# Kernel tuning notes

Measured on AMD Instinct MI355X. Metric: run time of the kernel, lower is better.

The kernel has to match this reference:

```python
import jax, jax.numpy as jnp
import numpy as np

ALPHA = 0.1      # weight on repulsion loss
NN_SIZE = 5      # k for knn (includes self, first neighbor dropped)
RADIUS = 0.07
H = 0.03
EPS = 1e-12


def _pairwise_sq(a, b):
    # a: (B, N, 3), b: (B, M, 3) -> (B, N, M) squared euclidean distances
    na = jnp.sum(a * a, axis=-1)[:, :, None]
    nb = jnp.sum(b * b, axis=-1)[:, None, :]
    return na + nb - 2.0 * jnp.einsum('bnc,bmc->bnm', a, b)


def setup_inputs() -> dict:
    key = jax.random.key(0)
    k1, k2, k3 = jax.random.split(key, 3)
    B, N = 8, 4096
    pred = jax.random.normal(k1, (B, N, 3), dtype=jnp.float32)
    gt = jax.random.normal(k2, (B, N, 3), dtype=jnp.float32)
    pcd_radius = jax.random.uniform(k3, (B, 1), dtype=jnp.float32)
    return {"pred": pred, "gt": gt, "pcd_radius": pcd_radius}


def reference(pred, gt, pcd_radius):
    # ---- Chamfer distance term (squared dists, as in ChamferDistance cuda op) ----
    d2 = _pairwise_sq(gt, pred)                  # (B, Ngt, Npred)
    cost_for = jnp.min(d2, axis=2)               # gt -> pred, (B, Ngt)
    cost_bac = jnp.min(d2, axis=1)               # pred -> gt, (B, Npred)
    cost = (0.8 * cost_for + 0.2 * cost_bac) / pcd_radius
    cd_loss = jnp.mean(cost)

    # ---- Repulsion (uniformity) term ----
    dpp = _pairwise_sq(pred, pred)               # (B, N, N)
    _, idx = jax.lax.top_k(-dpp, NN_SIZE)        # k nearest, (B, N, K); self is first
    idx = idx[:, :, 1:]                          # drop self, (B, N, K-1)
    # gather neighbors: (B, N, K-1, 3)
    neigh = jnp.take_along_axis(pred[:, None, :, :], idx[..., None], axis=2)
    diff = neigh - pred[:, :, None, :]
    dist2 = jnp.maximum(jnp.sum(diff * diff, axis=-1), EPS)  # (B, N, K-1)
    dist = jnp.sqrt(dist2)
    weight = jnp.exp(-dist2 / (H * H))
    uniform_loss = jnp.mean((RADIUS - dist) * weight)

    return cd_loss + ALPHA * uniform_loss
```

## Files before the change

### kernel.cpp

```cpp
#include <hip/hip_runtime.h>
#include <math.h>

#define THREADS 256
#define NWAVE 4
#define QB 128
#define TILE 1024
#define KSPLIT 2

#define MED3 __builtin_amdgcn_fmed3f

#define INS5(L0,L1,L2,L3,L4,C) do { float c_=(C);              \
    float n0_=fminf(L0,c_);                                    \
    float n1_=MED3(L0,L1,c_);                                  \
    float n2_=MED3(L1,L2,c_);                                  \
    float n3_=MED3(L2,L3,c_);                                  \
    float n4_=MED3(L3,L4,c_);                                  \
    L0=n0_; L1=n1_; L2=n2_; L3=n3_; L4=n4_; } while (0)

__device__ __forceinline__ float cdist(float qx,float qy,float qz,float4 t) {
    return fmaf(qx, t.x, fmaf(qy, t.y, fmaf(qz, t.z, t.w)));
}

__global__ __launch_bounds__(THREADS) void scan_kernel(
    const float* __restrict__ pred, const float* __restrict__ gt,
    const float* __restrict__ radius, float* __restrict__ acc,
    float* __restrict__ knnPart, int B, int N, int chunks, int knnItems)
{
    __shared__ float4 tile[TILE];
    __shared__ float part[NWAVE][QB][5];
    __shared__ float red[NWAVE];

    const float FLT_INF = 3.4e38f;

    int w = threadIdx.x >> 6, l = threadIdx.x & 63;

    int role, b, chunk, split = 0, tBegin, tEnd;
    if ((int)blockIdx.x < knnItems) {
        role = 2;
        int u = blockIdx.x;
        split = u % KSPLIT; u /= KSPLIT;
        chunk = u % chunks; b = u / chunks;
        int seg = (N + KSPLIT - 1) / KSPLIT;
        tBegin = split * seg; tEnd = min(tBegin + seg, N);
    } else {
        int u = blockIdx.x - knnItems;
        int perRole = B * chunks;
        role = u / perRole; u %= perRole;
        chunk = u % chunks; b = u / chunks;
        tBegin = 0; tEnd = N;
    }

    int qi0 = chunk * QB + l;
    int qi1 = qi0 + 64;
    const float* qb = (((role == 0) ? gt : pred)) + (size_t)b * N * 3;
    const float* tb = (((role == 1) ? gt : pred)) + (size_t)b * N * 3;

    float ax = 0.f, ay = 0.f, az = 0.f, bx = 0.f, by = 0.f, bz = 0.f;
    if (qi0 < N) { ax = qb[qi0*3]; ay = qb[qi0*3+1]; az = qb[qi0*3+2]; }
    if (qi1 < N) { bx = qb[qi1*3]; by = qb[qi1*3+1]; bz = qb[qi1*3+2]; }

    float mA0 = FLT_INF, mA1 = FLT_INF, mB0 = FLT_INF, mB1 = FLT_INF;
    float e0=FLT_INF,e1=FLT_INF,e2=FLT_INF,e3=FLT_INF,e4=FLT_INF;
    float o0=FLT_INF,o1=FLT_INF,o2=FLT_INF,o3=FLT_INF,o4=FLT_INF;

    for (int t0 = tBegin; t0 < tEnd; t0 += TILE) {
        int cnt = min(TILE, tEnd - t0);
        for (int k = threadIdx.x; k < cnt; k += THREADS) {
            float x = tb[(size_t)(t0 + k) * 3 + 0];
            float y = tb[(size_t)(t0 + k) * 3 + 1];
            float z = tb[(size_t)(t0 + k) * 3 + 2];
            float nb = fmaf(x, x, fmaf(y, y, z * z));
            tile[k] = make_float4(-2.f * x, -2.f * y, -2.f * z, nb);
        }
        __syncthreads();

        int seg = (cnt + NWAVE - 1) / NWAVE;
        int jb = w * seg, je = min(jb + seg, cnt);

        if (role < 2) {
            int j = jb;
            for (; j + 4 <= je; j += 4) {
                float4 t0v = tile[j], t1v = tile[j+1], t2v = tile[j+2], t3v = tile[j+3];
                mA0 = fminf(mA0, cdist(ax,ay,az,t0v));
                mB0 = fminf(mB0, cdist(bx,by,bz,t0v));
                mA1 = fminf(mA1, cdist(ax,ay,az,t1v));
                mB1 = fminf(mB1, cdist(bx,by,bz,t1v));
                mA0 = fminf(mA0, cdist(ax,ay,az,t2v));
                mB0 = fminf(mB0, cdist(bx,by,bz,t2v));
                mA1 = fminf(mA1, cdist(ax,ay,az,t3v));
                mB1 = fminf(mB1, cdist(bx,by,bz,t3v));
            }
            for (; j < je; ++j) {
                float4 t = tile[j];
                mA0 = fminf(mA0, cdist(ax,ay,az,t));
                mB0 = fminf(mB0, cdist(bx,by,bz,t));
            }
        } else {
            int j = jb;
            for (; j + 2 <= je; j += 2) {
                float4 t0v = tile[j], t1v = tile[j+1];
                float cA0 = cdist(ax,ay,az,t0v), cB0 = cdist(bx,by,bz,t0v);
                float cA1 = cdist(ax,ay,az,t1v), cB1 = cdist(bx,by,bz,t1v);
                INS5(e0,e1,e2,e3,e4, cA0);
                INS5(o0,o1,o2,o3,o4, cB0);
                INS5(e0,e1,e2,e3,e4, cA1);
                INS5(o0,o1,o2,o3,o4, cB1);
            }
            for (; j < je; ++j) {
                float4 t = tile[j];
                INS5(e0,e1,e2,e3,e4, cdist(ax,ay,az,t));
                INS5(o0,o1,o2,o3,o4, cdist(bx,by,bz,t));
            }
        }
        __syncthreads();
    }

    if (role < 2) {
        part[w][l][0]      = fminf(mA0, mA1);
        part[w][l + 64][0] = fminf(mB0, mB1);
    } else {
        part[w][l][0]=e0; part[w][l][1]=e1; part[w][l][2]=e2;
        part[w][l][3]=e3; part[w][l][4]=e4;
        part[w][l+64][0]=o0; part[w][l+64][1]=o1; part[w][l+64][2]=o2;
        part[w][l+64][3]=o3; part[w][l+64][4]=o4;
    }
    __syncthreads();

    if (role < 2) {
        float contrib = 0.f;
        if (threadIdx.x < QB) {
            int t = threadIdx.x;
            int q = chunk * QB + t;
            if (q < N) {
                float x = qb[q*3], y = qb[q*3+1], z = qb[q*3+2];
                float na = fmaf(x,x,fmaf(y,y,z*z));
                float best = fminf(fminf(part[0][t][0], part[1][t][0]),
                                   fminf(part[2][t][0], part[3][t][0]));
                float wgt = (role == 0) ? 0.8f : 0.2f;
                contrib = wgt * (na + best) / radius[b];
            }
        }
        #pragma unroll
        for (int off = 32; off > 0; off >>= 1) contrib += __shfl_down(contrib, off, 64);
        if (l == 0) red[w] = contrib;
        __syncthreads();
        if (threadIdx.x == 0) atomicAdd(&acc[0], red[0]+red[1]+red[2]+red[3]);
    } else {
        if (threadIdx.x < QB) {
            int t = threadIdx.x;
            int q = chunk * QB + t;
            if (q < N) {
                float s0=FLT_INF,s1=FLT_INF,s2=FLT_INF,s3=FLT_INF,s4=FLT_INF;
                #pragma unroll
                for (int ww = 0; ww < NWAVE; ++ww)
                    #pragma unroll
                    for (int k = 0; k < 5; ++k)
                        INS5(s0,s1,s2,s3,s4, part[ww][t][k]);
                float* kp = &knnPart[(((size_t)b * N + q) * KSPLIT + split) * 5];
                kp[0]=s0; kp[1]=s1; kp[2]=s2; kp[3]=s3; kp[4]=s4;
            }
        }
    }
}

__global__ __launch_bounds__(THREADS) void mergeB_kernel(
    const float* __restrict__ pred, const float* __restrict__ knnPart,
    float* __restrict__ acc, int B, int N)
{
    const float FLT_INF = 3.4e38f;
    const float RADIUS = 0.07f;
    const float INV_H2 = 1.0f / (0.03f * 0.03f);
    const float EPSV = 1e-12f;

    __shared__ float redu[NWAVE];

    int gid = blockIdx.x * THREADS + threadIdx.x;
    int BN = B * N;
    float uni = 0.f;

    if (gid < BN) {
        const float* qp = pred + (size_t)gid * 3;
        float x = qp[0], y = qp[1], z = qp[2];
        float na = fmaf(x,x,fmaf(y,y,z*z));
        const float* kp = &knnPart[(size_t)gid * KSPLIT * 5];
        float s0=FLT_INF,s1=FLT_INF,s2=FLT_INF,s3=FLT_INF,s4=FLT_INF;
        #pragma unroll
        for (int k = 0; k < KSPLIT * 5; ++k) INS5(s0,s1,s2,s3,s4, kp[k]);
        float ss[4] = {s1, s2, s3, s4};
        #pragma unroll
        for (int k = 0; k < 4; ++k) {
            float d2 = fmaxf(na + ss[k], EPSV);
            uni += (RADIUS - sqrtf(d2)) * __expf(-d2 * INV_H2);
        }
    }

    int w = threadIdx.x >> 6, l = threadIdx.x & 63;
    #pragma unroll
    for (int off = 32; off > 0; off >>= 1) uni += __shfl_down(uni, off, 64);
    if (l == 0) redu[w] = uni;
    __syncthreads();
    if (threadIdx.x == 0)
        atomicAdd(&acc[1], redu[0]+redu[1]+redu[2]+redu[3]);
}

__device__ __forceinline__ float sdist(float qx,float qy,float qz,float4 t) {
    return fmaf(-2.f, fmaf(qx,t.x,fmaf(qy,t.y,qz*t.z)), t.w);
}
__global__ __launch_bounds__(THREADS) void mono_kernel(
    const float* __restrict__ pred, const float* __restrict__ gt,
    const float* __restrict__ radius, float* __restrict__ acc,
    int B, int N, int chunksPerBatch)
{
    __shared__ float4 tgt[2048];
    __shared__ float part[NWAVE][128][5];
    __shared__ float naArr[128];
    __shared__ float red[NWAVE];
    const float FLT_INF = 3.4e38f;
    const float RADIUS = 0.07f;
    const float INV_H2 = 1.0f / (0.03f * 0.03f);
    const float EPSV = 1e-12f;

    int blocksPerRole = B * chunksPerBatch;
    int role  = blockIdx.x / blocksPerRole;
    int rem   = blockIdx.x % blocksPerRole;
    int b     = rem / chunksPerBatch;
    int chunk = rem % chunksPerBatch;
    int w = threadIdx.x >> 6, l = threadIdx.x & 63;
    int qi0 = chunk * 128 + l, qi1 = qi0 + 64;
    const float* qb = (((role == 0) ? gt : pred)) + (size_t)b * N * 3;
    const float* tb = (((role == 1) ? gt : pred)) + (size_t)b * N * 3;
    float q0x=0,q0y=0,q0z=0,q1x=0,q1y=0,q1z=0;
    if (qi0 < N) { q0x=qb[qi0*3]; q0y=qb[qi0*3+1]; q0z=qb[qi0*3+2]; }
    if (qi1 < N) { q1x=qb[qi1*3]; q1y=qb[qi1*3+1]; q1z=qb[qi1*3+2]; }
    float na0 = fmaf(q0x,q0x,fmaf(q0y,q0y,q0z*q0z));
    float na1 = fmaf(q1x,q1x,fmaf(q1y,q1y,q1z*q1z));
    if (w == 0) { naArr[l] = na0; naArr[l+64] = na1; }
    float mA=FLT_INF,mB=FLT_INF;
    float e0=FLT_INF,e1=FLT_INF,e2=FLT_INF,e3=FLT_INF,e4=FLT_INF;
    float o0=FLT_INF,o1=FLT_INF,o2=FLT_INF,o3=FLT_INF,o4=FLT_INF;
    for (int t0 = 0; t0 < N; t0 += 2048) {
        int cnt = min(2048, N - t0);
        for (int k = threadIdx.x; k < cnt; k += THREADS) {
            float x = tb[(size_t)(t0+k)*3], y = tb[(size_t)(t0+k)*3+1], z = tb[(size_t)(t0+k)*3+2];
            tgt[k] = make_float4(x,y,z,fmaf(x,x,fmaf(y,y,z*z)));
        }
        __syncthreads();
        int segsz = (cnt + NWAVE - 1)/NWAVE;
        int jb = w*segsz, je = min(jb+segsz, cnt);
        if (role < 2) {
            for (int j = jb; j < je; ++j) {
                float4 t = tgt[j];
                mA = fminf(mA, sdist(q0x,q0y,q0z,t));
                mB = fminf(mB, sdist(q1x,q1y,q1z,t));
            }
        } else {
            for (int j = jb; j < je; ++j) {
                float4 t = tgt[j];
                INS5(e0,e1,e2,e3,e4, sdist(q0x,q0y,q0z,t));
                INS5(o0,o1,o2,o3,o4, sdist(q1x,q1y,q1z,t));
            }
        }
        __syncthreads();
    }
    if (role < 2) { part[w][l][0]=mA; part[w][l+64][0]=mB; }
    else {
        part[w][l][0]=e0; part[w][l][1]=e1; part[w][l][2]=e2; part[w][l][3]=e3; part[w][l][4]=e4;
        part[w][l+64][0]=o0; part[w][l+64][1]=o1; part[w][l+64][2]=o2; part[w][l+64][3]=o3; part[w][l+64][4]=o4;
    }
    __syncthreads();
    float contrib = 0.f;
    int t = threadIdx.x;
    if (t < 128) {
        int q = chunk*128 + t;
        if (q < N) {
            float inv_r = 1.0f / radius[b];
            float na = naArr[t];
            if (role < 2) {
                float best = fminf(fminf(part[0][t][0],part[1][t][0]),
                                   fminf(part[2][t][0],part[3][t][0]));
                contrib = ((role==0)?0.8f:0.2f) * inv_r * (na + best);
            } else {
                float s0=FLT_INF,s1=FLT_INF,s2=FLT_INF,s3=FLT_INF,s4=FLT_INF;
                #pragma unroll
                for (int ww = 0; ww < NWAVE; ++ww)
                    #pragma unroll
                    for (int k = 0; k < 5; ++k)
                        INS5(s0,s1,s2,s3,s4, part[ww][t][k]);
                float ss[4] = {s1,s2,s3,s4};
                float s = 0.f;
                #pragma unroll
                for (int k = 0; k < 4; ++k) {
                    float d2 = fmaxf(na + ss[k], EPSV);
                    s += (RADIUS - sqrtf(d2)) * __expf(-d2 * INV_H2);
                }
                contrib = s;
            }
        }
    }
    #pragma unroll
    for (int off = 32; off > 0; off >>= 1) contrib += __shfl_down(contrib, off, 64);
    if (l == 0) red[w] = contrib;
    __syncthreads();
    if (threadIdx.x == 0)
        atomicAdd(&acc[role < 2 ? 0 : 1], red[0]+red[1]+red[2]+red[3]);
}

__global__ void upsample_final_kernel(const float* __restrict__ acc,
                                      float* __restrict__ out,
                                      float invCd, float invUni)
{
    out[0] = fmaf(acc[0], invCd, 0.1f * acc[1] * invUni);
}

extern "C" void kernel_launch(void* const* d_in, const int* in_sizes, int n_in,
                              void* d_out, int out_size, void* d_ws, size_t ws_size,
                              hipStream_t stream) {
    const float* pred   = (const float*)d_in[0];
    const float* gt     = (const float*)d_in[1];
    const float* radius = (const float*)d_in[2];
    float* out = (float*)d_out;
    float* acc = (float*)d_ws;

    int B = in_sizes[2];
    int N = in_sizes[0] / (3 * B);
    size_t BN = (size_t)B * N;

    hipMemsetAsync(acc, 0, 2 * sizeof(float), stream);

    size_t knnBytes = BN * KSPLIT * 5 * sizeof(float);
    size_t need = 64 + knnBytes;

    if (ws_size >= need) {
        float* knnPart = (float*)((char*)d_ws + 64);
        int chunks = (N + QB - 1) / QB;
        int knnItems  = B * chunks * KSPLIT;
        int chamItems = 2 * B * chunks;
        scan_kernel<<<knnItems + chamItems, THREADS, 0, stream>>>(
            pred, gt, radius, acc, knnPart, B, N, chunks, knnItems);
        int mb = (int)((BN + THREADS - 1) / THREADS);
        mergeB_kernel<<<mb, THREADS, 0, stream>>>(pred, knnPart, acc, B, N);
    } else {
        int chunksPerBatch = (N + 127) / 128;
        int blocks = 3 * B * chunksPerBatch;
        mono_kernel<<<blocks, THREADS, 0, stream>>>(pred, gt, radius, acc,
                                                    B, N, chunksPerBatch);
    }

    float invCd  = 1.0f / ((float)B * (float)N);
    float invUni = 1.0f / ((float)B * (float)N * 4.0f);
    upsample_final_kernel<<<1, 1, 0, stream>>>(acc, out, invCd, invUni);
}
```

Baseline: 72.93 us.

## Split chamfer and kNN target ranges further and merge partials in second kernel

Each chamfer query chunk now scans its targets in two halves, and kNN scans in four parts instead of two, which multiplies the number of scan blocks. Per-split chamfer minima go to a workspace buffer, and the merge kernel now also combines chamfer partials, applies the weights and radius, and reduces them. Tile size and the inner unroll are halved. The aim is more blocks to fill the GPU's compute units and shorter per-block scans, at the cost of extra global writes and a bigger merge pass.

```diff
diff --git a/kernel.cpp b/kernel.cpp
--- a/kernel.cpp
+++ b/kernel.cpp
@@ -4,8 +4,9 @@
 #define THREADS 256
 #define NWAVE 4
 #define QB 128
-#define TILE 1024
-#define KSPLIT 2
+#define TILE 512
+#define KSPLIT 4
+#define CSPLIT 2
 
 #define MED3 __builtin_amdgcn_fmed3f
 
@@ -23,18 +24,16 @@
 
 __global__ __launch_bounds__(THREADS) void scan_kernel(
     const float* __restrict__ pred, const float* __restrict__ gt,
-    const float* __restrict__ radius, float* __restrict__ acc,
-    float* __restrict__ knnPart, int B, int N, int chunks, int knnItems)
+    float* __restrict__ chamPart, float* __restrict__ knnPart,
+    int B, int N, int chunks, int knnItems)
 {
     __shared__ float4 tile[TILE];
     __shared__ float part[NWAVE][QB][5];
-    __shared__ float red[NWAVE];
 
     const float FLT_INF = 3.4e38f;
-
     int w = threadIdx.x >> 6, l = threadIdx.x & 63;
 
-    int role, b, chunk, split = 0, tBegin, tEnd;
+    int role, b, chunk, split, tBegin, tEnd;
     if ((int)blockIdx.x < knnItems) {
         role = 2;
         int u = blockIdx.x;
@@ -44,16 +43,19 @@
         tBegin = split * seg; tEnd = min(tBegin + seg, N);
     } else {
         int u = blockIdx.x - knnItems;
-        int perRole = B * chunks;
+        int perRole = B * chunks * CSPLIT;
         role = u / perRole; u %= perRole;
+        split = u % CSPLIT; u /= CSPLIT;
         chunk = u % chunks; b = u / chunks;
-        tBegin = 0; tEnd = N;
-    }
+        int seg = (N + CSPLIT - 1) / CSPLIT;
+        tBegin = split * seg; tEnd = min(tBegin + seg, N);
+    }
+
+    const float* qb = (((role == 0) ? gt : pred)) + (size_t)b * N * 3;
+    const float* tb = (((role == 1) ? gt : pred)) + (size_t)b * N * 3;
 
     int qi0 = chunk * QB + l;
     int qi1 = qi0 + 64;
-    const float* qb = (((role == 0) ? gt : pred)) + (size_t)b * N * 3;
-    const float* tb = (((role == 1) ? gt : pred)) + (size_t)b * N * 3;
 
     float ax = 0.f, ay = 0.f, az = 0.f, bx = 0.f, by = 0.f, bz = 0.f;
     if (qi0 < N) { ax = qb[qi0*3]; ay = qb[qi0*3+1]; az = qb[qi0*3+2]; }
@@ -69,8 +71,7 @@
             float x = tb[(size_t)(t0 + k) * 3 + 0];
             float y = tb[(size_t)(t0 + k) * 3 + 1];
             float z = tb[(size_t)(t0 + k) * 3 + 2];
-            float nb = fmaf(x, x, fmaf(y, y, z * z));
-            tile[k] = make_float4(-2.f * x, -2.f * y, -2.f * z, nb);
+            tile[k] = make_float4(-2.f*x, -2.f*y, -2.f*z, fmaf(x,x,fmaf(y,y,z*z)));
         }
         __syncthreads();
 
@@ -79,18 +80,14 @@
 
         if (role < 2) {
             int j = jb;
-            for (; j + 4 <= je; j += 4) {
-                float4 t0v = tile[j], t1v = tile[j+1], t2v = tile[j+2], t3v = tile[j+3];
+            for (; j + 2 <= je; j += 2) {
+                float4 t0v = tile[j], t1v = tile[j+1];
                 mA0 = fminf(mA0, cdist(ax,ay,az,t0v));
                 mB0 = fminf(mB0, cdist(bx,by,bz,t0v));
                 mA1 = fminf(mA1, cdist(ax,ay,az,t1v));
                 mB1 = fminf(mB1, cdist(bx,by,bz,t1v));
-                mA0 = fminf(mA0, cdist(ax,ay,az,t2v));
-                mB0 = fminf(mB0, cdist(bx,by,bz,t2v));
-                mA1 = fminf(mA1, cdist(ax,ay,az,t3v));
-                mB1 = fminf(mB1, cdist(bx,by,bz,t3v));
-            }
-            for (; j < je; ++j) {
+            }
+            if (j < je) {
                 float4 t = tile[j];
                 mA0 = fminf(mA0, cdist(ax,ay,az,t));
                 mB0 = fminf(mB0, cdist(bx,by,bz,t));
@@ -106,7 +103,7 @@
                 INS5(e0,e1,e2,e3,e4, cA1);
                 INS5(o0,o1,o2,o3,o4, cB1);
             }
-            for (; j < je; ++j) {
+            if (j < je) {
                 float4 t = tile[j];
                 INS5(e0,e1,e2,e3,e4, cdist(ax,ay,az,t));
                 INS5(o0,o1,o2,o3,o4, cdist(bx,by,bz,t));
@@ -126,30 +123,15 @@
     }
     __syncthreads();
 
-    if (role < 2) {
-        float contrib = 0.f;
-        if (threadIdx.x < QB) {
-            int t = threadIdx.x;
-            int q = chunk * QB + t;
-            if (q < N) {
-                float x = qb[q*3], y = qb[q*3+1], z = qb[q*3+2];
-                float na = fmaf(x,x,fmaf(y,y,z*z));
+    if (threadIdx.x < QB) {
+        int t = threadIdx.x;
+        int q = chunk * QB + t;
+        if (q < N) {
+            if (role < 2) {
                 float best = fminf(fminf(part[0][t][0], part[1][t][0]),
                                    fminf(part[2][t][0], part[3][t][0]));
-                float wgt = (role == 0) ? 0.8f : 0.2f;
-                contrib = wgt * (na + best) / radius[b];
-            }
-        }
-        #pragma unroll
-        for (int off = 32; off > 0; off >>= 1) contrib += __shfl_down(contrib, off, 64);
-        if (l == 0) red[w] = contrib;
-        __syncthreads();
-        if (threadIdx.x == 0) atomicAdd(&acc[0], red[0]+red[1]+red[2]+red[3]);
-    } else {
-        if (threadIdx.x < QB) {
-            int t = threadIdx.x;
-            int q = chunk * QB + t;
-            if (q < N) {
+                chamPart[(((size_t)role * B + b) * N + q) * CSPLIT + split] = best;
+            } else {
                 float s0=FLT_INF,s1=FLT_INF,s2=FLT_INF,s3=FLT_INF,s4=FLT_INF;
                 #pragma unroll
                 for (int ww = 0; ww < NWAVE; ++ww)
@@ -164,7 +146,9 @@
 }
 
 __global__ __launch_bounds__(THREADS) void mergeB_kernel(
-    const float* __restrict__ pred, const float* __restrict__ knnPart,
+    const float* __restrict__ pred, const float* __restrict__ gt,
+    const float* __restrict__ radius,
+    const float* __restrict__ chamPart, const float* __restrict__ knnPart,
     float* __restrict__ acc, int B, int N)
 {
     const float FLT_INF = 3.4e38f;
@@ -172,17 +156,29 @@
     const float INV_H2 = 1.0f / (0.03f * 0.03f);
     const float EPSV = 1e-12f;
 
-    __shared__ float redu[NWAVE];
+    __shared__ float redc[NWAVE], redu[NWAVE];
 
     int gid = blockIdx.x * THREADS + threadIdx.x;
     int BN = B * N;
-    float uni = 0.f;
-
-    if (gid < BN) {
-        const float* qp = pred + (size_t)gid * 3;
+    float cd = 0.f, uni = 0.f;
+
+    if (gid < 2 * BN) {
+        int role = gid / BN, q = gid % BN, b = q / N, qi = q % N;
+        const float* qp = ((role == 0) ? gt : pred) + (size_t)q * 3;
         float x = qp[0], y = qp[1], z = qp[2];
         float na = fmaf(x,x,fmaf(y,y,z*z));
-        const float* kp = &knnPart[(size_t)gid * KSPLIT * 5];
+        const float* cp = &chamPart[(size_t)gid * CSPLIT];
+        float m = cp[0];
+        #pragma unroll
+        for (int s = 1; s < CSPLIT; ++s) m = fminf(m, cp[s]);
+        float wgt = (role == 0) ? 0.8f : 0.2f;
+        cd = wgt * (na + m) / radius[b];
+    } else if (gid < 3 * BN) {
+        int q = gid - 2 * BN, b = q / N;
+        const float* qp = pred + (size_t)q * 3;
+        float x = qp[0], y = qp[1], z = qp[2];
+        float na = fmaf(x,x,fmaf(y,y,z*z));
+        const float* kp = &knnPart[(size_t)q * KSPLIT * 5];
         float s0=FLT_INF,s1=FLT_INF,s2=FLT_INF,s3=FLT_INF,s4=FLT_INF;
         #pragma unroll
         for (int k = 0; k < KSPLIT * 5; ++k) INS5(s0,s1,s2,s3,s4, kp[k]);
@@ -196,11 +192,16 @@
 
     int w = threadIdx.x >> 6, l = threadIdx.x & 63;
     #pragma unroll
-    for (int off = 32; off > 0; off >>= 1) uni += __shfl_down(uni, off, 64);
-    if (l == 0) redu[w] = uni;
+    for (int off = 32; off > 0; off >>= 1) {
+        cd  += __shfl_down(cd, off, 64);
+        uni += __shfl_down(uni, off, 64);
+    }
+    if (l == 0) { redc[w] = cd; redu[w] = uni; }
     __syncthreads();
-    if (threadIdx.x == 0)
+    if (threadIdx.x == 0) {
+        atomicAdd(&acc[0], redc[0]+redc[1]+redc[2]+redc[3]);
         atomicAdd(&acc[1], redu[0]+redu[1]+redu[2]+redu[3]);
+    }
 }
 
 __device__ __forceinline__ float sdist(float qx,float qy,float qz,float4 t) {
@@ -327,18 +328,21 @@
 
     hipMemsetAsync(acc, 0, 2 * sizeof(float), stream);
 
-    size_t knnBytes = BN * KSPLIT * 5 * sizeof(float);
-    size_t need = 64 + knnBytes;
+    size_t chamBytes = 2 * BN * CSPLIT * sizeof(float);
+    size_t knnBytes  = BN * KSPLIT * 5 * sizeof(float);
+    size_t need = 64 + chamBytes + knnBytes;
 
     if (ws_size >= need) {
-        float* knnPart = (float*)((char*)d_ws + 64);
+        float* chamPart = (float*)((char*)d_ws + 64);
+        float* knnPart  = chamPart + 2 * BN * CSPLIT;
         int chunks = (N + QB - 1) / QB;
         int knnItems  = B * chunks * KSPLIT;
-        int chamItems = 2 * B * chunks;
+        int chamItems = 2 * B * chunks * CSPLIT;
         scan_kernel<<<knnItems + chamItems, THREADS, 0, stream>>>(
-            pred, gt, radius, acc, knnPart, B, N, chunks, knnItems);
-        int mb = (int)((BN + THREADS - 1) / THREADS);
-        mergeB_kernel<<<mb, THREADS, 0, stream>>>(pred, knnPart, acc, B, N);
+            pred, gt, chamPart, knnPart, B, N, chunks, knnItems);
+        int mb = (int)((3 * BN + THREADS - 1) / THREADS);
+        mergeB_kernel<<<mb, THREADS, 0, stream>>>(pred, gt, radius,
+                                                  chamPart, knnPart, acc, B, N);
     } else {
         int chunksPerBatch = (N + 127) / 128;
         int blocks = 3 * B * chunksPerBatch;
```

Measured after the change: 88.71 us. +21.6%, slower.
